# Kernel tuning notes

Measured on AMD Instinct MI355X. Metric: run time of the kernel, lower is better.

Reference implementation:

```python
import jax, jax.numpy as jnp
import numpy as np

B, C, D, H, W = 2, 256, 16, 64, 64


def _conv1x1(x, w, b):
    # 1x1x1 Conv3d == pointwise channel matmul. x: [B,C,D,H,W], w: [Cout,Cin], b: [Cout]
    return jnp.einsum('bcdhw,oc->bodhw', x, w) + b[None, :, None, None, None]


def setup_inputs() -> dict:
    key = jax.random.key(0)
    ks = jax.random.split(key, 12)
    wscale = 1.0 / np.sqrt(C)  # keep pre-softmax logits in a sane range
    inp = {
        'eeg_input': jax.random.normal(ks[0], (B, C, D, H, W), jnp.float32),
        'image_input': jax.random.normal(ks[1], (B, C, D, H, W), jnp.float32),
        'q_w': jax.random.normal(ks[2], (C, C), jnp.float32) * wscale,
        'q_b': jnp.zeros((C,), jnp.float32),
        'k_w': jax.random.normal(ks[3], (C, C), jnp.float32) * wscale,
        'k_b': jnp.zeros((C,), jnp.float32),
        'v_w': jax.random.normal(ks[4], (C, C), jnp.float32) * wscale,
        'v_b': jnp.zeros((C,), jnp.float32),
        'attn_w': jax.random.normal(ks[5], (C, C), jnp.float32) * wscale,
        'attn_b': jnp.zeros((C,), jnp.float32),
        'out_w': jax.random.normal(ks[6], (C, C), jnp.float32) * wscale,
        'out_b': jnp.zeros((C,), jnp.float32),
    }
    return inp


def reference(eeg_input, image_input, q_w, q_b, k_w, k_b, v_w, v_b,
              attn_w, attn_b, out_w, out_b):
    q = _conv1x1(eeg_input, q_w, q_b)      # [B,C,D,H,W]
    k = _conv1x1(image_input, k_w, k_b)    # [B,C,D,H,W]
    v = _conv1x1(image_input, v_w, v_b)    # [B,C,D,H,W]
    # torch.matmul(q, k.transpose(-2,-1)): contract over W -> scores [B,C,D,H,H]
    scores = jax.nn.softmax(jnp.einsum('bcdhw,bcdxw->bcdhx', q, k), axis=-1)
    wv = jnp.einsum('bcdhx,bcdxw->bcdhw', scores, v)  # [B,C,D,H,W]
    a = jax.nn.relu(_conv1x1(wv, attn_w, attn_b))
    return jax.nn.relu(_conv1x1(a, out_w, out_b))
```

## Files before the change

### kernel.cpp

```cpp
#include <hip/hip_runtime.h>

#define CC   256
#define DHWC 65536
#define NBC  2

typedef __attribute__((ext_vector_type(8))) short bf16x8;
typedef __attribute__((ext_vector_type(4))) short bf16x4;
typedef __attribute__((ext_vector_type(4))) float f32x4;

__device__ __forceinline__ short f2bf(float x) {
    unsigned u = __builtin_bit_cast(unsigned, x);
    unsigned r = (u + 0x7fffu + ((u >> 16) & 1u)) >> 16;
    return (short)r;
}
__device__ __forceinline__ float bf2f(short h) {
    unsigned u = ((unsigned)(unsigned short)h) << 16;
    return __builtin_bit_cast(float, u);
}

__device__ __forceinline__ int swz(int r, int c) {
    return (r * 128 + c * 2) ^ ((r & 7) << 4);
}
__device__ __forceinline__ int vswz(int r, int c) {
    return (r * 128 + c * 2) ^ (((r ^ (r >> 3)) & 7) << 4);
}
__device__ __forceinline__ int swz512(int s, int k) {
    return (s * 512 + k * 2) ^ ((s & 7) << 4);
}
__device__ __forceinline__ int swz256(int r, int s) {
    return (r * 256 + s * 2) ^ ((r & 7) << 4);
}
__device__ __forceinline__ int swzf(int r, int c) {
    return (r * 512 + c * 4) ^ ((r & 7) << 4);
}
__device__ __forceinline__ int swzf64(int r, int c) {
    return (r * 256 + c * 4) ^ ((r & 7) << 4);
}

__global__ void prep_w_kernel(const float* __restrict__ q_w, const float* __restrict__ k_w,
                              const float* __restrict__ v_w, const float* __restrict__ attn_w,
                              const float* __restrict__ out_w, short* __restrict__ wsp)
{
    const int l  = threadIdx.x;
    const int fo = blockIdx.x;
    const int t  = blockIdx.y;
    const int m  = blockIdx.z;
    const float* w = (m == 0) ? q_w : (m == 1) ? k_w : (m == 2) ? v_w
                   : (m == 3) ? attn_w : out_w;
    short* whi = wsp + (size_t)m * 131072;
    short* wlo = whi + 65536;

    const int o = fo * 16 + (l & 15);
    const int k = t * 32 + (l >> 4) * 8;

    bf16x8 hv, lv;
    #pragma unroll
    for (int r = 0; r < 8; ++r) {
        const float x = w[o * 256 + k + r];
        const short h = f2bf(x);
        hv[r] = h;
        lv[r] = f2bf(x - bf2f(h));
    }
    const int idx = (fo * 8 + t) * 64 + l;
    *(bf16x8*)(whi + idx * 8) = hv;
    *(bf16x8*)(wlo + idx * 8) = lv;
}

__global__ __launch_bounds__(1024, 4) void conv_mfma_kernel(
    const float* __restrict__ x, const short* __restrict__ whi,
    const short* __restrict__ wlo, const float* __restrict__ bias,
    float* __restrict__ out)
{
    __shared__ char lds[65536];

    const int tid  = threadIdx.x;
    const int lane = tid & 63;
    const int wave = tid >> 6;
    const size_t boff = (size_t)blockIdx.y * ((size_t)CC * DHWC);
    const int sT = blockIdx.x * 128;
    const float* xb = x + boff + sT;
    const bf16x8* whf = (const bf16x8*)whi;
    const bf16x8* wlf = (const bf16x8*)wlo;

    f32x4 acc[8];
    #pragma unroll
    for (int j = 0; j < 8; ++j) acc[j] = (f32x4){0.f, 0.f, 0.f, 0.f};

    const int s_l = tid & 127;
    const int k8  = tid >> 7;

    float xr[8];
    #pragma unroll
    for (int r = 0; r < 8; ++r)
        xr[r] = xb[(size_t)(k8 * 8 + r) * DHWC + s_l];
    {
        bf16x8 hv, lv;
        #pragma unroll
        for (int r = 0; r < 8; ++r) {
            const short h = f2bf(xr[r]);
            hv[r] = h;
            lv[r] = f2bf(xr[r] - bf2f(h));
        }
        const int off = swz(s_l, k8 * 8);
        *(bf16x8*)(lds + off) = hv;
        *(bf16x8*)(lds + 16384 + off) = lv;
    }

    #pragma unroll
    for (int t = 0; t < 4; ++t) {
        if (t < 3) {
            #pragma unroll
            for (int r = 0; r < 8; ++r)
                xr[r] = xb[(size_t)((t + 1) * 64 + k8 * 8 + r) * DHWC + s_l];
        }
        __syncthreads();

        const char* bhib = lds + (t & 1) * 32768;
        const char* blob = bhib + 16384;
        #pragma unroll
        for (int kk = 0; kk < 2; ++kk) {
            const int idx = (wave * 8 + 2 * t + kk) * 64 + lane;
            const bf16x8 a1h = whf[idx];
            const bf16x8 a1l = wlf[idx];
            #pragma unroll
            for (int j = 0; j < 8; ++j) {
                const int s = j * 16 + (lane & 15);
                const int k = kk * 32 + (lane >> 4) * 8;
                const bf16x8 bh = *(const bf16x8*)(bhib + swz(s, k));
                const bf16x8 bl = *(const bf16x8*)(blob + swz(s, k));
                f32x4 c = acc[j];
                c = __builtin_amdgcn_mfma_f32_16x16x32_bf16(a1h, bh, c, 0, 0, 0);
                c = __builtin_amdgcn_mfma_f32_16x16x32_bf16(a1h, bl, c, 0, 0, 0);
                c = __builtin_amdgcn_mfma_f32_16x16x32_bf16(a1l, bh, c, 0, 0, 0);
                acc[j] = c;
            }
        }

        if (t < 3) {
            bf16x8 hv, lv;
            #pragma unroll
            for (int r = 0; r < 8; ++r) {
                const short h = f2bf(xr[r]);
                hv[r] = h;
                lv[r] = f2bf(xr[r] - bf2f(h));
            }
            const int off = ((t + 1) & 1) * 32768 + swz(s_l, k8 * 8);
            *(bf16x8*)(lds + off) = hv;
            *(bf16x8*)(lds + 16384 + off) = lv;
        }
    }

    float* ob = out + boff + sT;
    const int n_l = lane & 15;
    const int m4  = (lane >> 4) * 4;
    #pragma unroll
    for (int h = 0; h < 2; ++h) {
        __syncthreads();
        if ((wave >> 3) == h) {
            #pragma unroll
            for (int r = 0; r < 4; ++r) {
                const int o = wave * 16 + m4 + r;
                const float bv = bias[o];
                const int lr = o & 127;
                #pragma unroll
                for (int j = 0; j < 8; ++j)
                    *(float*)(lds + swzf(lr, j * 16 + n_l)) = acc[j][r] + bv;
            }
        }
        __syncthreads();
        #pragma unroll
        for (int it = 0; it < 4; ++it) {
            const int lr = it * 32 + (tid >> 5);
            const int c4 = (tid & 31) * 4;
            const float4 vv = *(const float4*)(lds + swzf(lr, c4));
            *(float4*)(ob + (size_t)(h * 128 + lr) * DHWC + c4) = vv;
        }
    }
}

__global__ __launch_bounds__(1024, 4) void kv_conv_kernel(
    const float* __restrict__ img,
    const short* __restrict__ wkhi, const short* __restrict__ wklo,
    const short* __restrict__ wvhi, const short* __restrict__ wvlo,
    const float* __restrict__ kb, const float* __restrict__ vb,
    float* __restrict__ kout, short* __restrict__ vout)
{
    __shared__ char lds[65536];

    const int tid  = threadIdx.x;
    const int lane = tid & 63;
    const int wave = tid >> 6;
    const size_t boff = (size_t)blockIdx.y * ((size_t)CC * DHWC);
    const int sT = blockIdx.x * 128;
    const float* xb = img + boff + sT;
    const bf16x8* wkhf = (const bf16x8*)wkhi;
    const bf16x8* wklf = (const bf16x8*)wklo;
    const bf16x8* wvhf = (const bf16x8*)wvhi;
    const bf16x8* wvlf = (const bf16x8*)wvlo;

    f32x4 acck[8], accv[8];
    #pragma unroll
    for (int j = 0; j < 8; ++j) {
        acck[j] = (f32x4){0.f, 0.f, 0.f, 0.f};
        accv[j] = (f32x4){0.f, 0.f, 0.f, 0.f};
    }

    const int s_l = tid & 127;
    const int k8  = tid >> 7;

    float xr[8];
    #pragma unroll
    for (int r = 0; r < 8; ++r)
        xr[r] = xb[(size_t)(k8 * 8 + r) * DHWC + s_l];
    {
        bf16x8 hv, lv;
        #pragma unroll
        for (int r = 0; r < 8; ++r) {
            const short h = f2bf(xr[r]);
            hv[r] = h;
            lv[r] = f2bf(xr[r] - bf2f(h));
        }
        const int off = swz(s_l, k8 * 8);
        *(bf16x8*)(lds + off) = hv;
        *(bf16x8*)(lds + 16384 + off) = lv;
    }

    #pragma unroll
    for (int t = 0; t < 4; ++t) {
        if (t < 3) {
            #pragma unroll
            for (int r = 0; r < 8; ++r)
                xr[r] = xb[(size_t)((t + 1) * 64 + k8 * 8 + r) * DHWC + s_l];
        }
        __syncthreads();

        const char* bhib = lds + (t & 1) * 32768;
        const char* blob = bhib + 16384;
        #pragma unroll
        for (int kk = 0; kk < 2; ++kk) {
            const int idx = (wave * 8 + 2 * t + kk) * 64 + lane;
            const bf16x8 akh = wkhf[idx];
            const bf16x8 akl = wklf[idx];
            const bf16x8 avh = wvhf[idx];
            const bf16x8 avl = wvlf[idx];
            #pragma unroll
            for (int j = 0; j < 8; ++j) {
                const int s = j * 16 + (lane & 15);
                const int k = kk * 32 + (lane >> 4) * 8;
                const bf16x8 bh = *(const bf16x8*)(bhib + swz(s, k));
                const bf16x8 bl = *(const bf16x8*)(blob + swz(s, k));
                f32x4 c = acck[j];
                c = __builtin_amdgcn_mfma_f32_16x16x32_bf16(akh, bh, c, 0, 0, 0);
                c = __builtin_amdgcn_mfma_f32_16x16x32_bf16(akh, bl, c, 0, 0, 0);
                c = __builtin_amdgcn_mfma_f32_16x16x32_bf16(akl, bh, c, 0, 0, 0);
                acck[j] = c;
                f32x4 d = accv[j];
                d = __builtin_amdgcn_mfma_f32_16x16x32_bf16(avh, bh, d, 0, 0, 0);
                d = __builtin_amdgcn_mfma_f32_16x16x32_bf16(avh, bl, d, 0, 0, 0);
                d = __builtin_amdgcn_mfma_f32_16x16x32_bf16(avl, bh, d, 0, 0, 0);
                accv[j] = d;
            }
        }

        if (t < 3) {
            bf16x8 hv, lv;
            #pragma unroll
            for (int r = 0; r < 8; ++r) {
                const short h = f2bf(xr[r]);
                hv[r] = h;
                lv[r] = f2bf(xr[r] - bf2f(h));
            }
            const int off = ((t + 1) & 1) * 32768 + swz(s_l, k8 * 8);
            *(bf16x8*)(lds + off) = hv;
            *(bf16x8*)(lds + 16384 + off) = lv;
        }
    }

    const int n_l = lane & 15;
    const int m4  = (lane >> 4) * 4;

    float* ko = kout + boff + sT;
    #pragma unroll
    for (int h = 0; h < 2; ++h) {
        __syncthreads();
        if ((wave >> 3) == h) {
            #pragma unroll
            for (int r = 0; r < 4; ++r) {
                const int o = wave * 16 + m4 + r;
                const float kbv = kb[o];
                const int lr = o & 127;
                #pragma unroll
                for (int j = 0; j < 8; ++j)
                    *(float*)(lds + swzf(lr, j * 16 + n_l)) = acck[j][r] + kbv;
            }
        }
        __syncthreads();
        #pragma unroll
        for (int it = 0; it < 4; ++it) {
            const int lr = it * 32 + (tid >> 5);
            const int c4 = (tid & 31) * 4;
            const float4 vv = *(const float4*)(lds + swzf(lr, c4));
            *(float4*)(ko + (size_t)(h * 128 + lr) * DHWC + c4) = vv;
        }
    }

    __syncthreads();
    #pragma unroll
    for (int r = 0; r < 4; ++r) {
        const int o = wave * 16 + m4 + r;
        const float vbv = vb[o];
        #pragma unroll
        for (int j = 0; j < 8; ++j)
            *(short*)(lds + swz256(o, j * 16 + n_l)) = f2bf(accv[j][r] + vbv);
    }
    __syncthreads();
    short* vo = vout + boff + sT;
    #pragma unroll
    for (int it = 0; it < 4; ++it) {
        const int row = it * 64 + wave * 4 + (lane >> 4);
        const int sc  = (lane & 15) * 8;
        const bf16x8 v8 = *(const bf16x8*)(lds + swz256(row, sc));
        *(bf16x8*)(vo + (size_t)row * DHWC + sc) = v8;
    }
}

template<int WVM>
__global__ __launch_bounds__(256, 4) void attn_mfma_kernel(
    const float* q, const float* __restrict__ kg,
    const short* __restrict__ vsh, float* wvf, short* __restrict__ wvs)
{
    __shared__ char lds[40960];
    const int QHI = 0, QLO = 8192, KHI = 16384, KLO = 24576, VT = 32768;

    const int tid  = threadIdx.x;
    const int lane = tid & 63;
    const int wsx  = tid >> 6;
    const size_t base = (size_t)blockIdx.x * 4096;

    {
        const int r  = tid >> 2;
        const int cb = (tid & 3) * 16;
        #pragma unroll
        for (int half = 0; half < 2; ++half) {
            const int c = cb + half * 8;
            const float4 qa = *(const float4*)(q  + base + r * 64 + c);
            const float4 qb = *(const float4*)(q  + base + r * 64 + c + 4);
            const float4 ka = *(const float4*)(kg + base + r * 64 + c);
            const float4 kb = *(const float4*)(kg + base + r * 64 + c + 4);
            bf16x8 qh, ql, kh, kl;
            #pragma unroll
            for (int e = 0; e < 4; ++e) {
                float xq = ((const float*)&qa)[e];
                short h = f2bf(xq); qh[e] = h; ql[e] = f2bf(xq - bf2f(h));
                xq = ((const float*)&qb)[e];
                h = f2bf(xq); qh[e + 4] = h; ql[e + 4] = f2bf(xq - bf2f(h));
                float xk = ((const float*)&ka)[e];
                h = f2bf(xk); kh[e] = h; kl[e] = f2bf(xk - bf2f(h));
                xk = ((const float*)&kb)[e];
                h = f2bf(xk); kh[e + 4] = h; kl[e + 4] = f2bf(xk - bf2f(h));
            }
            const int off = swz(r, c);
            *(bf16x8*)(lds + QHI + off) = qh;
            *(bf16x8*)(lds + QLO + off) = ql;
            *(bf16x8*)(lds + KHI + off) = kh;
            *(bf16x8*)(lds + KLO + off) = kl;
        }
        const short* vpl = vsh + base;
        const int x0 = (tid >> 4) * 4;
        const int w0 = (tid & 15) * 4;
        bf16x4 vr[4];
        #pragma unroll
        for (int i = 0; i < 4; ++i)
            vr[i] = *(const bf16x4*)(vpl + (x0 + i) * 64 + w0);
        #pragma unroll
        for (int j = 0; j < 4; ++j) {
            bf16x4 tv;
            #pragma unroll
            for (int i = 0; i < 4; ++i) tv[i] = vr[i][j];
            *(bf16x4*)(lds + VT + vswz(w0 + j, x0)) = tv;
        }
    }
    __syncthreads();

    f32x4 acc[4];
    #pragma unroll
    for (int j = 0; j < 4; ++j) acc[j] = (f32x4){0.f, 0.f, 0.f, 0.f};

    const int arow = wsx * 16 + (lane & 15);
    #pragma unroll
    for (int kk = 0; kk < 2; ++kk) {
        const int kcol = kk * 32 + (lane >> 4) * 8;
        const bf16x8 aqh = *(const bf16x8*)(lds + QHI + swz(arow, kcol));
        const bf16x8 aql = *(const bf16x8*)(lds + QLO + swz(arow, kcol));
        #pragma unroll
        for (int j = 0; j < 4; ++j) {
            const int brow = j * 16 + (lane & 15);
            const bf16x8 bkh = *(const bf16x8*)(lds + KHI + swz(brow, kcol));
            const bf16x8 bkl = *(const bf16x8*)(lds + KLO + swz(brow, kcol));
            f32x4 c = acc[j];
            c = __builtin_amdgcn_mfma_f32_16x16x32_bf16(aqh, bkh, c, 0, 0, 0);
            c = __builtin_amdgcn_mfma_f32_16x16x32_bf16(aqh, bkl, c, 0, 0, 0);
            c = __builtin_amdgcn_mfma_f32_16x16x32_bf16(aql, bkh, c, 0, 0, 0);
            acc[j] = c;
        }
    }

    float p[4][4], invs[4];
    #pragma unroll
    for (int r = 0; r < 4; ++r) {
        float m = fmaxf(fmaxf(acc[0][r], acc[1][r]), fmaxf(acc[2][r], acc[3][r]));
        m = fmaxf(m, __shfl_xor(m, 1));
        m = fmaxf(m, __shfl_xor(m, 2));
        m = fmaxf(m, __shfl_xor(m, 4));
        m = fmaxf(m, __shfl_xor(m, 8));
        float s = 0.f;
        #pragma unroll
        for (int j = 0; j < 4; ++j) { p[j][r] = __expf(acc[j][r] - m); s += p[j][r]; }
        s += __shfl_xor(s, 1);
        s += __shfl_xor(s, 2);
        s += __shfl_xor(s, 4);
        s += __shfl_xor(s, 8);
        invs[r] = 1.f / s;
    }

    __syncthreads();

    #pragma unroll
    for (int r = 0; r < 4; ++r) {
        const int row = wsx * 16 + (lane >> 4) * 4 + r;
        #pragma unroll
        for (int j = 0; j < 4; ++j) {
            const int col = j * 16 + (lane & 15);
            *(short*)(lds + QHI + swz(row, col)) = f2bf(p[j][r]);
        }
    }
    __syncthreads();

    f32x4 o_[4];
    #pragma unroll
    for (int j = 0; j < 4; ++j) o_[j] = (f32x4){0.f, 0.f, 0.f, 0.f};

    #pragma unroll
    for (int kk = 0; kk < 2; ++kk) {
        const int kcol = kk * 32 + (lane >> 4) * 8;
        const bf16x8 aph = *(const bf16x8*)(lds + QHI + swz(arow, kcol));
        #pragma unroll
        for (int j = 0; j < 4; ++j) {
            const int brow = j * 16 + (lane & 15);
            const bf16x8 bvh = *(const bf16x8*)(lds + VT + vswz(brow, kcol));
            o_[j] = __builtin_amdgcn_mfma_f32_16x16x32_bf16(aph, bvh, o_[j], 0, 0, 0);
        }
    }

    if (WVM == 0) {
        __syncthreads();
        #pragma unroll
        for (int r = 0; r < 4; ++r) {
            const int h = wsx * 16 + (lane >> 4) * 4 + r;
            #pragma unroll
            for (int j = 0; j < 4; ++j)
                *(float*)(lds + swzf64(h, j * 16 + (lane & 15))) = o_[j][r] * invs[r];
        }
        __syncthreads();
        #pragma unroll
        for (int it = 0; it < 4; ++it) {
            const int row = it * 16 + (tid >> 4);
            const int c4  = (tid & 15) * 4;
            const float4 vv = *(const float4*)(lds + swzf64(row, c4));
            *(float4*)(wvf + base + (size_t)row * 64 + c4) = vv;
        }
    } else {
        __syncthreads();
        #pragma unroll
        for (int r = 0; r < 4; ++r) {
            const int h = wsx * 16 + (lane >> 4) * 4 + r;
            #pragma unroll
            for (int j = 0; j < 4; ++j)
                *(short*)(lds + QHI + swz(h, j * 16 + (lane & 15))) = f2bf(o_[j][r] * invs[r]);
        }
        __syncthreads();
        #pragma unroll
        for (int it = 0; it < 4; ++it) {
            const int row = it * 16 + (tid >> 4);
            const int sc  = (tid & 15) * 4;
            bf16x4 v4;
            v4 = *(const bf16x4*)(lds + QHI + ((row * 128 + sc * 2) ^ ((row & 7) << 4)));
            *(bf16x4*)(wvs + base + (size_t)row * 64 + sc) = v4;
        }
    }
}

template<int IM>
__global__ __launch_bounds__(1024, 4) void tail_fused_kernel(
    const float* __restrict__ xf, const short* __restrict__ xs,
    const short* __restrict__ w1hi, const short* __restrict__ w1lo,
    const float* __restrict__ b1,
    const short* __restrict__ w2hi, const short* __restrict__ w2lo,
    const float* __restrict__ b2,
    float* __restrict__ out)
{
    __shared__ char lds[65536];

    const int tid  = threadIdx.x;
    const int lane = tid & 63;
    const int wave = tid >> 6;
    const size_t boff = (size_t)blockIdx.y * ((size_t)CC * DHWC);
    const int sT = blockIdx.x * 128;
    const bf16x8* w1hf = (const bf16x8*)w1hi;
    const bf16x8* w1lf = (const bf16x8*)w1lo;

    f32x4 acc[8];
    #pragma unroll
    for (int j = 0; j < 8; ++j) acc[j] = (f32x4){0.f, 0.f, 0.f, 0.f};

    const int s_l = tid & 127;
    const int k8  = tid >> 7;
    const float* xbf = xf + boff + sT;
    const short* xbs = xs + boff + sT;

    float xr[8];
    short sr[8];
    if (IM == 0) {
        #pragma unroll
        for (int r = 0; r < 8; ++r)
            xr[r] = xbf[(size_t)(k8 * 8 + r) * DHWC + s_l];
        bf16x8 hv, lv;
        #pragma unroll
        for (int r = 0; r < 8; ++r) {
            const short h = f2bf(xr[r]);
            hv[r] = h;
            lv[r] = f2bf(xr[r] - bf2f(h));
        }
        const int off = swz(s_l, k8 * 8);
        *(bf16x8*)(lds + off) = hv;
        *(bf16x8*)(lds + 16384 + off) = lv;
    } else {
        #pragma unroll
        for (int r = 0; r < 8; ++r)
            sr[r] = xbs[(size_t)(k8 * 8 + r) * DHWC + s_l];
        bf16x8 hv;
        #pragma unroll
        for (int r = 0; r < 8; ++r) hv[r] = sr[r];
        *(bf16x8*)(lds + swz(s_l, k8 * 8)) = hv;
    }

    #pragma unroll
    for (int t = 0; t < 4; ++t) {
        if (t < 3) {
            if (IM == 0) {
                #pragma unroll
                for (int r = 0; r < 8; ++r)
                    xr[r] = xbf[(size_t)((t + 1) * 64 + k8 * 8 + r) * DHWC + s_l];
            } else {
                #pragma unroll
                for (int r = 0; r < 8; ++r)
                    sr[r] = xbs[(size_t)((t + 1) * 64 + k8 * 8 + r) * DHWC + s_l];
            }
        }
        __syncthreads();

        const char* bhib = lds + (t & 1) * (IM == 0 ? 32768 : 16384);
        const char* blob = bhib + 16384;
        #pragma unroll
        for (int kk = 0; kk < 2; ++kk) {
            const int idx = (wave * 8 + 2 * t + kk) * 64 + lane;
            const bf16x8 a1h = w1hf[idx];
            const bf16x8 a1l = w1lf[idx];
            #pragma unroll
            for (int j = 0; j < 8; ++j) {
                const int s = j * 16 + (lane & 15);
                const int k = kk * 32 + (lane >> 4) * 8;
                const bf16x8 bh = *(const bf16x8*)(bhib + swz(s, k));
                f32x4 c = acc[j];
                c = __builtin_amdgcn_mfma_f32_16x16x32_bf16(a1h, bh, c, 0, 0, 0);
                c = __builtin_amdgcn_mfma_f32_16x16x32_bf16(a1l, bh, c, 0, 0, 0);
                if (IM == 0) {
                    const bf16x8 bl = *(const bf16x8*)(blob + swz(s, k));
                    c = __builtin_amdgcn_mfma_f32_16x16x32_bf16(a1h, bl, c, 0, 0, 0);
                }
                acc[j] = c;
            }
        }

        if (t < 3) {
            const int off = ((t + 1) & 1) * (IM == 0 ? 32768 : 16384) + swz(s_l, k8 * 8);
            if (IM == 0) {
                bf16x8 hv, lv;
                #pragma unroll
                for (int r = 0; r < 8; ++r) {
                    const short h = f2bf(xr[r]);
                    hv[r] = h;
                    lv[r] = f2bf(xr[r] - bf2f(h));
                }
                *(bf16x8*)(lds + off) = hv;
                *(bf16x8*)(lds + 16384 + off) = lv;
            } else {
                bf16x8 hv;
                #pragma unroll
                for (int r = 0; r < 8; ++r) hv[r] = sr[r];
                *(bf16x8*)(lds + off) = hv;
            }
        }
    }

    __syncthreads();
    {
        const int m4 = (lane >> 4) * 4;
        #pragma unroll
        for (int r = 0; r < 4; ++r) {
            const int o = wave * 16 + m4 + r;
            const float bv = b1[o];
            #pragma unroll
            for (int j = 0; j < 8; ++j) {
                const int s = j * 16 + (lane & 15);
                *(short*)(lds + swz512(s, o)) = f2bf(fmaxf(acc[j][r] + bv, 0.f));
            }
        }
    }
    __syncthreads();

    f32x4 acc2[8];
    #pragma unroll
    for (int j = 0; j < 8; ++j) acc2[j] = (f32x4){0.f, 0.f, 0.f, 0.f};

    const bf16x8* w2hf = (const bf16x8*)w2hi;
    const bf16x8* w2lf = (const bf16x8*)w2lo;
    #pragma unroll
    for (int t2 = 0; t2 < 8; ++t2) {
        const int idx = (wave * 8 + t2) * 64 + lane;
        const bf16x8 a2h = w2hf[idx];
        const bf16x8 a2l = w2lf[idx];
        #pragma unroll
        for (int j = 0; j < 8; ++j) {
            const int s = j * 16 + (lane & 15);
            const int k = t2 * 32 + (lane >> 4) * 8;
            const bf16x8 bh = *(const bf16x8*)(lds + swz512(s, k));
            f32x4 c = acc2[j];
            c = __builtin_amdgcn_mfma_f32_16x16x32_bf16(a2h, bh, c, 0, 0, 0);
            c = __builtin_amdgcn_mfma_f32_16x16x32_bf16(a2l, bh, c, 0, 0, 0);
            acc2[j] = c;
        }
    }

    float* ob = out + boff + sT;
    const int n_l = lane & 15;
    const int m4  = (lane >> 4) * 4;
    #pragma unroll
    for (int h = 0; h < 2; ++h) {
        __syncthreads();
        if ((wave >> 3) == h) {
            #pragma unroll
            for (int r = 0; r < 4; ++r) {
                const int o = wave * 16 + m4 + r;
                const float bv = b2[o];
                const int lr = o & 127;
                #pragma unroll
                for (int j = 0; j < 8; ++j)
                    *(float*)(lds + swzf(lr, j * 16 + n_l)) = fmaxf(acc2[j][r] + bv, 0.f);
            }
        }
        __syncthreads();
        #pragma unroll
        for (int it = 0; it < 4; ++it) {
            const int lr = it * 32 + (tid >> 5);
            const int c4 = (tid & 31) * 4;
            const float4 vv = *(const float4*)(lds + swzf(lr, c4));
            *(float4*)(ob + (size_t)(h * 128 + lr) * DHWC + c4) = vv;
        }
    }
}

extern "C" void kernel_launch(void* const* d_in, const int* in_sizes, int n_in,
                              void* d_out, int out_size, void* d_ws, size_t ws_size,
                              hipStream_t stream)
{
    const float* eeg    = (const float*)d_in[0];
    const float* img    = (const float*)d_in[1];
    const float* q_w    = (const float*)d_in[2];
    const float* q_b    = (const float*)d_in[3];
    const float* k_w    = (const float*)d_in[4];
    const float* k_b    = (const float*)d_in[5];
    const float* v_w    = (const float*)d_in[6];
    const float* v_b    = (const float*)d_in[7];
    const float* attn_w = (const float*)d_in[8];
    const float* attn_b = (const float*)d_in[9];
    const float* out_w  = (const float*)d_in[10];
    const float* out_b  = (const float*)d_in[11];

    const size_t N = (size_t)NBC * CC * DHWC;
    float* qbuf = (float*)d_ws;
    float* kbuf = qbuf + N;
    const size_t need_rich = 4 * N + 4 * N + 2 * N + (size_t)5 * 131072 * 2;
    const bool rich = (ws_size >= need_rich);
    short* wvs = rich ? (short*)(kbuf + N) : (short*)nullptr;
    short* wsp = rich ? (wvs + N) : (short*)(kbuf + N);
    short* vsh  = (short*)d_out;
    float* outp = (float*)d_out;

    prep_w_kernel<<<dim3(16, 8, 5), dim3(64), 0, stream>>>(
        q_w, k_w, v_w, attn_w, out_w, wsp);

    const dim3 cgrid(DHWC / 128, NBC);

    conv_mfma_kernel<<<cgrid, dim3(1024), 0, stream>>>(
        eeg, wsp, wsp + 65536, q_b, qbuf);

    kv_conv_kernel<<<cgrid, dim3(1024), 0, stream>>>(
        img, wsp + 131072, wsp + 131072 + 65536,
        wsp + 2 * 131072, wsp + 2 * 131072 + 65536,
        k_b, v_b, kbuf, vsh);

    if (rich) {
        attn_mfma_kernel<1><<<dim3(NBC * CC * 16), dim3(256), 0, stream>>>(
            qbuf, kbuf, vsh, (float*)nullptr, wvs);
        tail_fused_kernel<1><<<cgrid, dim3(1024), 0, stream>>>(
            (const float*)nullptr, wvs,
            wsp + 3 * 131072, wsp + 3 * 131072 + 65536, attn_b,
            wsp + 4 * 131072, wsp + 4 * 131072 + 65536, out_b, outp);
    } else {
        attn_mfma_kernel<0><<<dim3(NBC * CC * 16), dim3(256), 0, stream>>>(
            qbuf, kbuf, vsh, qbuf, (short*)nullptr);
        tail_fused_kernel<0><<<cgrid, dim3(1024), 0, stream>>>(
            qbuf, (const short*)nullptr,
            wsp + 3 * 131072, wsp + 3 * 131072 + 65536, attn_b,
            wsp + 4 * 131072, wsp + 4 * 131072 + 65536, out_b, outp);
    }
}
```

Measured before the change: 400.0 us.

## Deepen global-load prefetch to two stages in pointwise conv kernels

The three channel-matmul kernels now keep two register sets of prefetched input rows, issuing global loads two K-steps ahead instead of one, so load latency has more MFMA work to hide behind. The attention kernel's Q/K staging loop is also reshaped to use float4 loads with bf16x4 LDS stores in a more coalesced row mapping. The deeper prefetch raises register pressure and could reduce occupancy.

```diff
diff --git a/kernel.cpp b/kernel.cpp
--- a/kernel.cpp
+++ b/kernel.cpp
@@ -89,32 +89,28 @@
     const int s_l = tid & 127;
     const int k8  = tid >> 7;
 
-    float xr[8];
-    #pragma unroll
-    for (int r = 0; r < 8; ++r)
-        xr[r] = xb[(size_t)(k8 * 8 + r) * DHWC + s_l];
-    {
-        bf16x8 hv, lv;
-        #pragma unroll
-        for (int r = 0; r < 8; ++r) {
-            const short h = f2bf(xr[r]);
-            hv[r] = h;
-            lv[r] = f2bf(xr[r] - bf2f(h));
-        }
-        const int off = swz(s_l, k8 * 8);
-        *(bf16x8*)(lds + off) = hv;
-        *(bf16x8*)(lds + 16384 + off) = lv;
-    }
+    float xr2[2][8];
+    #define QLOAD(SET, STEP) { \
+        _Pragma("unroll") \
+        for (int r = 0; r < 8; ++r) \
+            xr2[SET][r] = xb[(size_t)((STEP) * 64 + k8 * 8 + r) * DHWC + s_l]; }
+    #define QSTAGE(SET, BUF) { \
+        bf16x8 hv, lv; \
+        _Pragma("unroll") \
+        for (int r = 0; r < 8; ++r) { \
+            const short h = f2bf(xr2[SET][r]); \
+            hv[r] = h; \
+            lv[r] = f2bf(xr2[SET][r] - bf2f(h)); } \
+        const int off = (BUF) * 32768 + swz(s_l, k8 * 8); \
+        *(bf16x8*)(lds + off) = hv; \
+        *(bf16x8*)(lds + 16384 + off) = lv; }
+
+    QLOAD(0, 0) QSTAGE(0, 0)
+    QLOAD(0, 1) QLOAD(1, 2)
 
     #pragma unroll
     for (int t = 0; t < 4; ++t) {
-        if (t < 3) {
-            #pragma unroll
-            for (int r = 0; r < 8; ++r)
-                xr[r] = xb[(size_t)((t + 1) * 64 + k8 * 8 + r) * DHWC + s_l];
-        }
-        __syncthreads();
-
+        __syncthreads();
         const char* bhib = lds + (t & 1) * 32768;
         const char* blob = bhib + 16384;
         #pragma unroll
@@ -135,20 +131,13 @@
                 acc[j] = c;
             }
         }
-
         if (t < 3) {
-            bf16x8 hv, lv;
-            #pragma unroll
-            for (int r = 0; r < 8; ++r) {
-                const short h = f2bf(xr[r]);
-                hv[r] = h;
-                lv[r] = f2bf(xr[r] - bf2f(h));
-            }
-            const int off = ((t + 1) & 1) * 32768 + swz(s_l, k8 * 8);
-            *(bf16x8*)(lds + off) = hv;
-            *(bf16x8*)(lds + 16384 + off) = lv;
-        }
-    }
+            QSTAGE((t & 1), ((t + 1) & 1))
+            if (t == 0) QLOAD(0, 3)
+        }
+    }
+    #undef QLOAD
+    #undef QSTAGE
 
     float* ob = out + boff + sT;
     const int n_l = lane & 15;
@@ -208,32 +197,28 @@
     const int s_l = tid & 127;
     const int k8  = tid >> 7;
 
-    float xr[8];
-    #pragma unroll
-    for (int r = 0; r < 8; ++r)
-        xr[r] = xb[(size_t)(k8 * 8 + r) * DHWC + s_l];
-    {
-        bf16x8 hv, lv;
-        #pragma unroll
-        for (int r = 0; r < 8; ++r) {
-            const short h = f2bf(xr[r]);
-            hv[r] = h;
-            lv[r] = f2bf(xr[r] - bf2f(h));
-        }
-        const int off = swz(s_l, k8 * 8);
-        *(bf16x8*)(lds + off) = hv;
-        *(bf16x8*)(lds + 16384 + off) = lv;
-    }
+    float xr2[2][8];
+    #define QLOAD(SET, STEP) { \
+        _Pragma("unroll") \
+        for (int r = 0; r < 8; ++r) \
+            xr2[SET][r] = xb[(size_t)((STEP) * 64 + k8 * 8 + r) * DHWC + s_l]; }
+    #define QSTAGE(SET, BUF) { \
+        bf16x8 hv, lv; \
+        _Pragma("unroll") \
+        for (int r = 0; r < 8; ++r) { \
+            const short h = f2bf(xr2[SET][r]); \
+            hv[r] = h; \
+            lv[r] = f2bf(xr2[SET][r] - bf2f(h)); } \
+        const int off = (BUF) * 32768 + swz(s_l, k8 * 8); \
+        *(bf16x8*)(lds + off) = hv; \
+        *(bf16x8*)(lds + 16384 + off) = lv; }
+
+    QLOAD(0, 0) QSTAGE(0, 0)
+    QLOAD(0, 1) QLOAD(1, 2)
 
     #pragma unroll
     for (int t = 0; t < 4; ++t) {
-        if (t < 3) {
-            #pragma unroll
-            for (int r = 0; r < 8; ++r)
-                xr[r] = xb[(size_t)((t + 1) * 64 + k8 * 8 + r) * DHWC + s_l];
-        }
-        __syncthreads();
-
+        __syncthreads();
         const char* bhib = lds + (t & 1) * 32768;
         const char* blob = bhib + 16384;
         #pragma unroll
@@ -261,20 +246,13 @@
                 accv[j] = d;
             }
         }
-
         if (t < 3) {
-            bf16x8 hv, lv;
-            #pragma unroll
-            for (int r = 0; r < 8; ++r) {
-                const short h = f2bf(xr[r]);
-                hv[r] = h;
-                lv[r] = f2bf(xr[r] - bf2f(h));
-            }
-            const int off = ((t + 1) & 1) * 32768 + swz(s_l, k8 * 8);
-            *(bf16x8*)(lds + off) = hv;
-            *(bf16x8*)(lds + 16384 + off) = lv;
-        }
-    }
+            QSTAGE((t & 1), ((t + 1) & 1))
+            if (t == 0) QLOAD(0, 3)
+        }
+    }
+    #undef QLOAD
+    #undef QSTAGE
 
     const int n_l = lane & 15;
     const int m4  = (lane >> 4) * 4;
@@ -338,32 +316,25 @@
     const size_t base = (size_t)blockIdx.x * 4096;
 
     {
-        const int r  = tid >> 2;
-        const int cb = (tid & 3) * 16;
-        #pragma unroll
-        for (int half = 0; half < 2; ++half) {
-            const int c = cb + half * 8;
+        #pragma unroll
+        for (int it = 0; it < 4; ++it) {
+            const int r = it * 16 + (tid >> 4);
+            const int c = (tid & 15) * 4;
             const float4 qa = *(const float4*)(q  + base + r * 64 + c);
-            const float4 qb = *(const float4*)(q  + base + r * 64 + c + 4);
             const float4 ka = *(const float4*)(kg + base + r * 64 + c);
-            const float4 kb = *(const float4*)(kg + base + r * 64 + c + 4);
-            bf16x8 qh, ql, kh, kl;
+            bf16x4 qh, ql, kh, kl;
             #pragma unroll
             for (int e = 0; e < 4; ++e) {
-                float xq = ((const float*)&qa)[e];
+                const float xq = ((const float*)&qa)[e];
                 short h = f2bf(xq); qh[e] = h; ql[e] = f2bf(xq - bf2f(h));
-                xq = ((const float*)&qb)[e];
-                h = f2bf(xq); qh[e + 4] = h; ql[e + 4] = f2bf(xq - bf2f(h));
-                float xk = ((const float*)&ka)[e];
+                const float xk = ((const float*)&ka)[e];
                 h = f2bf(xk); kh[e] = h; kl[e] = f2bf(xk - bf2f(h));
-                xk = ((const float*)&kb)[e];
-                h = f2bf(xk); kh[e + 4] = h; kl[e + 4] = f2bf(xk - bf2f(h));
             }
             const int off = swz(r, c);
-            *(bf16x8*)(lds + QHI + off) = qh;
-            *(bf16x8*)(lds + QLO + off) = ql;
-            *(bf16x8*)(lds + KHI + off) = kh;
-            *(bf16x8*)(lds + KLO + off) = kl;
+            *(bf16x4*)(lds + QHI + off) = qh;
+            *(bf16x4*)(lds + QLO + off) = ql;
+            *(bf16x4*)(lds + KHI + off) = kh;
+            *(bf16x4*)(lds + KLO + off) = kl;
         }
         const short* vpl = vsh + base;
         const int x0 = (tid >> 4) * 4;
@@ -518,47 +489,42 @@
     const float* xbf = xf + boff + sT;
     const short* xbs = xs + boff + sT;
 
-    float xr[8];
-    short sr[8];
-    if (IM == 0) {
-        #pragma unroll
-        for (int r = 0; r < 8; ++r)
-            xr[r] = xbf[(size_t)(k8 * 8 + r) * DHWC + s_l];
-        bf16x8 hv, lv;
-        #pragma unroll
-        for (int r = 0; r < 8; ++r) {
-            const short h = f2bf(xr[r]);
-            hv[r] = h;
-            lv[r] = f2bf(xr[r] - bf2f(h));
-        }
-        const int off = swz(s_l, k8 * 8);
-        *(bf16x8*)(lds + off) = hv;
-        *(bf16x8*)(lds + 16384 + off) = lv;
-    } else {
-        #pragma unroll
-        for (int r = 0; r < 8; ++r)
-            sr[r] = xbs[(size_t)(k8 * 8 + r) * DHWC + s_l];
-        bf16x8 hv;
-        #pragma unroll
-        for (int r = 0; r < 8; ++r) hv[r] = sr[r];
-        *(bf16x8*)(lds + swz(s_l, k8 * 8)) = hv;
-    }
+    float xr2[2][8];
+    short sr2[2][8];
+    #define TLOAD(SET, STEP) { \
+        if (IM == 0) { \
+            _Pragma("unroll") \
+            for (int r = 0; r < 8; ++r) \
+                xr2[SET][r] = xbf[(size_t)((STEP) * 64 + k8 * 8 + r) * DHWC + s_l]; \
+        } else { \
+            _Pragma("unroll") \
+            for (int r = 0; r < 8; ++r) \
+                sr2[SET][r] = xbs[(size_t)((STEP) * 64 + k8 * 8 + r) * DHWC + s_l]; \
+        } }
+    #define TSTAGE(SET, BUF) { \
+        if (IM == 0) { \
+            bf16x8 hv, lv; \
+            _Pragma("unroll") \
+            for (int r = 0; r < 8; ++r) { \
+                const short h = f2bf(xr2[SET][r]); \
+                hv[r] = h; \
+                lv[r] = f2bf(xr2[SET][r] - bf2f(h)); } \
+            const int off = (BUF) * 32768 + swz(s_l, k8 * 8); \
+            *(bf16x8*)(lds + off) = hv; \
+            *(bf16x8*)(lds + 16384 + off) = lv; \
+        } else { \
+            bf16x8 hv; \
+            _Pragma("unroll") \
+            for (int r = 0; r < 8; ++r) hv[r] = sr2[SET][r]; \
+            *(bf16x8*)(lds + (BUF) * 16384 + swz(s_l, k8 * 8)) = hv; \
+        } }
+
+    TLOAD(0, 0) TSTAGE(0, 0)
+    TLOAD(0, 1) TLOAD(1, 2)
 
     #pragma unroll
     for (int t = 0; t < 4; ++t) {
-        if (t < 3) {
-            if (IM == 0) {
-                #pragma unroll
-                for (int r = 0; r < 8; ++r)
-                    xr[r] = xbf[(size_t)((t + 1) * 64 + k8 * 8 + r) * DHWC + s_l];
-            } else {
-                #pragma unroll
-                for (int r = 0; r < 8; ++r)
-                    sr[r] = xbs[(size_t)((t + 1) * 64 + k8 * 8 + r) * DHWC + s_l];
-            }
-        }
-        __syncthreads();
-
+        __syncthreads();
         const char* bhib = lds + (t & 1) * (IM == 0 ? 32768 : 16384);
         const char* blob = bhib + 16384;
         #pragma unroll
@@ -581,27 +547,13 @@
                 acc[j] = c;
             }
         }
-
         if (t < 3) {
-            const int off = ((t + 1) & 1) * (IM == 0 ? 32768 : 16384) + swz(s_l, k8 * 8);
-            if (IM == 0) {
-                bf16x8 hv, lv;
-                #pragma unroll
-                for (int r = 0; r < 8; ++r) {
-                    const short h = f2bf(xr[r]);
-                    hv[r] = h;
-                    lv[r] = f2bf(xr[r] - bf2f(h));
-                }
-                *(bf16x8*)(lds + off) = hv;
-                *(bf16x8*)(lds + 16384 + off) = lv;
-            } else {
-                bf16x8 hv;
-                #pragma unroll
-                for (int r = 0; r < 8; ++r) hv[r] = sr[r];
-                *(bf16x8*)(lds + off) = hv;
-            }
-        }
-    }
+            TSTAGE((t & 1), ((t + 1) & 1))
+            if (t == 0) TLOAD(0, 3)
+        }
+    }
+    #undef TLOAD
+    #undef TSTAGE
 
     __syncthreads();
     {
```

After: 416.9 us. 1.04x slower.
